# Performance work log

Measured on AMD Instinct MI355X. Metric: run time of the kernel, lower is better.

## Reference

```python
import jax, jax.numpy as jnp
import numpy as np

N = 50000
E = 1600000
IN_C = 128
HID = 64
OUT_C = 64
EPS = 1e-5
NEG_SLOPE = 0.01  # nn.LeakyReLU default


def setup_inputs() -> dict:
    key = jax.random.key(0)
    ks = jax.random.split(key, 8)
    x = jax.random.normal(ks[0], (N, IN_C), dtype=jnp.float32)
    x_e = jnp.zeros((1,), dtype=jnp.float32)  # unused by the module
    edge_index = jax.random.randint(ks[1], (2, E), 0, N, dtype=jnp.int64)
    # Parameters (torch default-ish init scale)
    s1 = 1.0 / np.sqrt(IN_C)
    W1 = jax.random.uniform(ks[2], (HID, IN_C), jnp.float32, -s1, s1)
    b1 = jax.random.uniform(ks[3], (HID,), jnp.float32, -s1, s1)
    gamma = jnp.ones((HID,), jnp.float32)
    beta = jnp.zeros((HID,), jnp.float32)
    s2 = 1.0 / np.sqrt(HID)
    W2 = jax.random.uniform(ks[4], (OUT_C, HID), jnp.float32, -s2, s2)
    b2 = jax.random.uniform(ks[5], (OUT_C,), jnp.float32, -s2, s2)
    return {"x": x, "x_e": x_e, "edge_index": edge_index,
            "W1": W1, "b1": b1, "gamma": gamma, "beta": beta,
            "W2": W2, "b2": b2}


def reference(x, x_e, edge_index, W1, b1, gamma, beta, W2, b2):
    # dropout: identity in eval mode
    h = jax.nn.leaky_relu(x @ W1.T + b1, negative_slope=NEG_SLOPE)  # [N, HID]
    # LayerNorm over last dim
    mu = jnp.mean(h, axis=-1, keepdims=True)
    var = jnp.mean(jnp.square(h - mu), axis=-1, keepdims=True)
    h = (h - mu) * jax.lax.rsqrt(var + EPS) * gamma + beta
    # gather over src edges, scatter-min into dst nodes
    src, dst = edge_index[0], edge_index[1]
    agg = jax.ops.segment_min(h[src], dst, num_segments=N)  # [N, HID]
    # nodes with no incoming edge: segment_min -> +inf; PyG fills 0
    agg = jnp.where(jnp.isinf(agg), 0.0, agg)
    out = agg @ W2.T + b2  # [N, OUT_C]
    return out
```

## Files before the change

kernel.cpp:

```cpp
#include <hip/hip_runtime.h>
#include <hip/hip_fp16.h>
#include <cstdint>
#include <math.h>

#define IN_C 128
#define HID 64
#define OUT_C 64
#define EPS_LN 1e-5f
#define NEG_SLOPE 0.01f

#define NBUCKET 1024
#define ROWS 49
#define CAP 2048
#define EPB 4096

typedef __attribute__((ext_vector_type(8))) short short8;
typedef __attribute__((ext_vector_type(4))) float f32x4;
typedef __attribute__((ext_vector_type(2))) _Float16 f16x2;
typedef __attribute__((ext_vector_type(8))) _Float16 f16x8;

__device__ __forceinline__ unsigned pack_hi(float f0, float f1) {
    return (__float_as_uint(f0) >> 16) | (__float_as_uint(f1) & 0xFFFF0000u);
}
__device__ __forceinline__ float hi_part(float f) {
    return __uint_as_float(__float_as_uint(f) & 0xFFFF0000u);
}
__device__ __forceinline__ unsigned hmin2u(unsigned a, unsigned b) {
    union { unsigned u; f16x2 v; } ua, ub, r;
    ua.u = a; ub.u = b;
    r.v = __builtin_elementwise_min(ua.v, ub.v);
    return r.u;
}

__global__ __launch_bounds__(512) void mlp_and_scatter_kernel(
    const float* __restrict__ x, const float* __restrict__ W1,
    const float* __restrict__ b1, const float* __restrict__ gamma,
    const float* __restrict__ beta, unsigned short* __restrict__ h16,
    const int* __restrict__ ei, unsigned* __restrict__ cursor ,
    unsigned* __restrict__ pairs, int N, int E, int NB_MLP, int NB_SCAT)
{
    __shared__ __align__(16) unsigned smem[12928];

    const int tid = threadIdx.x;
    const int bx  = blockIdx.x;

    const int nmin2 = 2 * min(NB_MLP, NB_SCAT);
    bool do_mlp; int id;
    if (bx < nmin2) { do_mlp = (bx & 1) == 0; id = bx >> 1; }
    else {
        int rr = bx - nmin2;
        do_mlp = (NB_MLP > NB_SCAT);
        id = (nmin2 >> 1) + rr;
    }

    if (do_mlp) {
        unsigned* whi = smem;
        unsigned* wlo = smem + 4352;
        unsigned short* hT = (unsigned short*)(smem + 8704);

        if (tid < 256) {
            int r = tid >> 2, q = tid & 3;
            const float4* wr4 = (const float4*)(W1 + r * IN_C + q * 32);
#pragma unroll
            for (int p = 0; p < 8; ++p) {
                float4 f = wr4[p];
                whi[r * 68 + q * 16 + 2 * p]     = pack_hi(f.x, f.y);
                whi[r * 68 + q * 16 + 2 * p + 1] = pack_hi(f.z, f.w);
                wlo[r * 68 + q * 16 + 2 * p]     = pack_hi(f.x - hi_part(f.x), f.y - hi_part(f.y));
                wlo[r * 68 + q * 16 + 2 * p + 1] = pack_hi(f.z - hi_part(f.z), f.w - hi_part(f.w));
            }
        }
        __syncthreads();

        const int lane = tid & 63;
        const int w    = tid >> 6;
        const int col  = lane & 15;
        const int g    = lane >> 4;
        const int nodeBase0 = id * 128;
        const int nodeBase  = nodeBase0 + w * 16;

        f32x4 acc[4];
#pragma unroll
        for (int t = 0; t < 4; ++t) acc[t] = (f32x4){0.f, 0.f, 0.f, 0.f};

        const int nodeCl = min(nodeBase + col, N - 1);

#pragma unroll
        for (int ks = 0; ks < 4; ++ks) {
            const float* xp = x + (size_t)nodeCl * IN_C + ks * 32 + g * 8;
            float4 fa = *(const float4*)xp;
            float4 fb = *(const float4*)(xp + 4);
            float f[8] = {fa.x, fa.y, fa.z, fa.w, fb.x, fb.y, fb.z, fb.w};
            union { unsigned u[4]; short8 s; } Ah, Al;
#pragma unroll
            for (int p = 0; p < 4; ++p) {
                float f0 = f[2 * p], f1 = f[2 * p + 1];
                Ah.u[p] = pack_hi(f0, f1);
                Al.u[p] = pack_hi(f0 - hi_part(f0), f1 - hi_part(f1));
            }
#pragma unroll
            for (int t = 0; t < 4; ++t) {
                short8 Bh = *(const short8*)&whi[(t * 16 + col) * 68 + ks * 16 + g * 4];
                short8 Bl = *(const short8*)&wlo[(t * 16 + col) * 68 + ks * 16 + g * 4];
                acc[t] = __builtin_amdgcn_mfma_f32_16x16x32_bf16(Ah.s, Bh, acc[t], 0, 0, 0);
                acc[t] = __builtin_amdgcn_mfma_f32_16x16x32_bf16(Ah.s, Bl, acc[t], 0, 0, 0);
                acc[t] = __builtin_amdgcn_mfma_f32_16x16x32_bf16(Al.s, Bh, acc[t], 0, 0, 0);
            }
        }

        float b1v[4], gv[4], bv[4];
#pragma unroll
        for (int t = 0; t < 4; ++t) {
            b1v[t] = b1[t * 16 + col];
            gv[t]  = gamma[t * 16 + col];
            bv[t]  = beta[t * 16 + col];
        }
        float val[4][4];
#pragma unroll
        for (int t = 0; t < 4; ++t)
#pragma unroll
            for (int r = 0; r < 4; ++r) {
                float v = acc[t][r] + b1v[t];
                val[t][r] = v > 0.f ? v : v * NEG_SLOPE;
            }

        float s[4], q[4];
#pragma unroll
        for (int r = 0; r < 4; ++r) {
            s[r] = val[0][r] + val[1][r] + val[2][r] + val[3][r];
            q[r] = fmaf(val[0][r], val[0][r],
                   fmaf(val[1][r], val[1][r],
                   fmaf(val[2][r], val[2][r], val[3][r] * val[3][r])));
        }
#pragma unroll
        for (int off = 1; off < 16; off <<= 1) {
#pragma unroll
            for (int r = 0; r < 4; ++r) {
                s[r] += __shfl_xor(s[r], off, 64);
                q[r] += __shfl_xor(q[r], off, 64);
            }
        }
        float mu[4], rstd[4];
#pragma unroll
        for (int r = 0; r < 4; ++r) {
            mu[r] = s[r] * (1.f / 64.f);
            float var = q[r] * (1.f / 64.f) - mu[r] * mu[r];
            rstd[r] = rsqrtf(var + EPS_LN);
        }
#pragma unroll
        for (int t = 0; t < 4; ++t)
#pragma unroll
            for (int r = 0; r < 4; ++r) {
                float hn = (val[t][r] - mu[r]) * rstd[r] * gv[t] + bv[t];
                int nodeL = w * 16 + g * 4 + r;
                hT[nodeL * 66 + t * 16 + col] = __half_as_ushort(__float2half(hn));
            }
        __syncthreads();

        {
            int nodeL = tid >> 2, part = tid & 3;
            int node = nodeBase0 + nodeL;
            if (node < N) {
                const unsigned* hrow = (const unsigned*)hT;
                unsigned tmp[8];
#pragma unroll
                for (int i = 0; i < 8; ++i) tmp[i] = hrow[nodeL * 33 + part * 8 + i];
                unsigned* gp = (unsigned*)h16 + (size_t)node * 32 + part * 8;
                *(uint4*)gp       = (uint4){tmp[0], tmp[1], tmp[2], tmp[3]};
                *(uint4*)(gp + 4) = (uint4){tmp[4], tmp[5], tmp[6], tmp[7]};
            }
        }
    } else {
        unsigned* staged    = smem;
        unsigned short* bof = (unsigned short*)(smem + 4096);
        unsigned* hist      = smem + 6144;
        unsigned* run_start = smem + 7168;
        unsigned* c2        = smem + 8192;
        unsigned* gbase     = smem + 9216;
        unsigned* wsum      = smem + 10240;

        const int base = id * EPB;
        const int lane = tid & 63;
        const int wv   = tid >> 6;

        hist[tid] = 0;
        hist[tid + 512] = 0;
        __syncthreads();

        unsigned pk[8];
        unsigned short bk[8];
#pragma unroll
        for (int k = 0; k < 8; ++k) {
            int e = base + k * 512 + tid;
            if (e < E) {
                unsigned src = (unsigned)ei[e];
                unsigned dst = (unsigned)ei[E + e];
                unsigned b = dst & (NBUCKET - 1);
                pk[k] = src | ((dst >> 10) << 16);
                bk[k] = (unsigned short)b;
                atomicAdd(&hist[b], 1u);
            } else {
                bk[k] = 0xFFFFu;
            }
        }
        __syncthreads();

        unsigned sA = hist[2 * tid], sB = hist[2 * tid + 1];
        unsigned sv = sA + sB;
        unsigned inc = sv;
#pragma unroll
        for (int off = 1; off < 64; off <<= 1) {
            unsigned u = __shfl_up(inc, (unsigned)off, 64);
            if (lane >= off) inc += u;
        }
        if (lane == 63) wsum[wv] = inc;
        __syncthreads();
        unsigned wbase = 0;
        for (int i = 0; i < wv; ++i) wbase += wsum[i];
        unsigned excl = wbase + inc - sv;

        run_start[2 * tid] = excl;
        run_start[2 * tid + 1] = excl + sA;
        c2[2 * tid] = excl;
        c2[2 * tid + 1] = excl + sA;
        if (sA) gbase[2 * tid] = atomicAdd(&cursor[(2 * tid) * 16], sA);
        if (sB) gbase[2 * tid + 1] = atomicAdd(&cursor[(2 * tid + 1) * 16], sB);
        __syncthreads();

#pragma unroll
        for (int k = 0; k < 8; ++k) {
            if (bk[k] != 0xFFFFu) {
                unsigned pos = atomicAdd(&c2[bk[k]], 1u);
                staged[pos] = pk[k];
                bof[pos] = bk[k];
            }
        }
        __syncthreads();

        int total = min(EPB, E - base);
        for (int i = tid; i < total; i += 512) {
            unsigned b = bof[i];
            unsigned local = gbase[b] + ((unsigned)i - run_start[b]);
            if (local < CAP) pairs[(size_t)b * CAP + local] = staged[i];
        }
    }
}

__global__ __launch_bounds__(512) void bucket_reduce_gemm_kernel(
    const unsigned* __restrict__ hp ,
    const unsigned* __restrict__ cursor, const unsigned* __restrict__ pairs,
    const float* __restrict__ W2, const float* __restrict__ b2,
    float* __restrict__ out, int N)
{
    __shared__ unsigned rec_sorted[CAP];
    __shared__ unsigned accP[64 * 36];
    __shared__ unsigned w2h[64 * 36];
    __shared__ unsigned rhist[64], rstart[64], rc[64];

    const int tid  = threadIdx.x;
    const int lane = tid & 63;
    const int wid  = tid >> 6;
    const unsigned b = blockIdx.x;
    const unsigned INITV = 0x7C007C00u;

    if (tid < 64) rhist[tid] = 0;
    for (int i = tid; i < 64 * 36; i += 512) accP[i] = INITV;
    for (int i = tid; i < 64 * 32; i += 512) {
        int n = i >> 5, p = i & 31;
        float f0 = W2[n * 64 + 2 * p], f1 = W2[n * 64 + 2 * p + 1];
        unsigned u0 = (unsigned)__half_as_ushort(__float2half(f0));
        unsigned u1 = (unsigned)__half_as_ushort(__float2half(f1));
        w2h[n * 36 + p] = u0 | (u1 << 16);
    }

    const unsigned cnt = min(cursor[b * 16], (unsigned)CAP);
    unsigned myrec[4];
#pragma unroll
    for (int k = 0; k < 4; ++k) {
        unsigned i = (unsigned)tid + k * 512;
        myrec[k] = (i < cnt) ? pairs[(size_t)b * CAP + i] : 0xFFFFFFFFu;
    }
    __syncthreads();

#pragma unroll
    for (int k = 0; k < 4; ++k)
        if (myrec[k] != 0xFFFFFFFFu) atomicAdd(&rhist[myrec[k] >> 16], 1u);
    __syncthreads();

    if (wid == 0) {
        unsigned v = (lane < ROWS) ? rhist[lane] : 0u;
        unsigned inc = v;
#pragma unroll
        for (int off = 1; off < 64; off <<= 1) {
            unsigned u = __shfl_up(inc, (unsigned)off, 64);
            if (lane >= off) inc += u;
        }
        if (lane < ROWS) { rstart[lane] = inc - v; rc[lane] = inc - v; }
    }
    __syncthreads();

#pragma unroll
    for (int k = 0; k < 4; ++k)
        if (myrec[k] != 0xFFFFFFFFu) {
            unsigned pos = atomicAdd(&rc[myrec[k] >> 16], 1u);
            rec_sorted[pos] = myrec[k];
        }
    __syncthreads();

    const unsigned sub = (unsigned)(lane >> 3);
    const unsigned cg  = (unsigned)(lane & 7);
    for (int r = wid; r < ROWS; r += 8) {
        unsigned L = rhist[r];
        if (L == 0) continue;
        unsigned st = rstart[r];
        uint4 acc  = {INITV, INITV, INITV, INITV};
        uint4 acc2 = {INITV, INITV, INITV, INITV};
        for (unsigned bb = 0; bb < L; bb += 16) {
            unsigned k1 = min(bb + sub, L - 1);
            unsigned k2 = min(bb + 8 + sub, L - 1);
            unsigned n1 = rec_sorted[st + k1] & 0xFFFFu;
            unsigned n2 = rec_sorted[st + k2] & 0xFFFFu;
            uint4 v1 = *(const uint4*)(hp + (size_t)n1 * 32 + cg * 4);
            uint4 v2 = *(const uint4*)(hp + (size_t)n2 * 32 + cg * 4);
            acc.x  = hmin2u(acc.x,  v1.x); acc.y  = hmin2u(acc.y,  v1.y);
            acc.z  = hmin2u(acc.z,  v1.z); acc.w  = hmin2u(acc.w,  v1.w);
            acc2.x = hmin2u(acc2.x, v2.x); acc2.y = hmin2u(acc2.y, v2.y);
            acc2.z = hmin2u(acc2.z, v2.z); acc2.w = hmin2u(acc2.w, v2.w);
        }
        acc.x = hmin2u(acc.x, acc2.x); acc.y = hmin2u(acc.y, acc2.y);
        acc.z = hmin2u(acc.z, acc2.z); acc.w = hmin2u(acc.w, acc2.w);
#pragma unroll
        for (int off = 8; off < 64; off <<= 1) {
            acc.x = hmin2u(acc.x, (unsigned)__shfl_xor((int)acc.x, off, 64));
            acc.y = hmin2u(acc.y, (unsigned)__shfl_xor((int)acc.y, off, 64));
            acc.z = hmin2u(acc.z, (unsigned)__shfl_xor((int)acc.z, off, 64));
            acc.w = hmin2u(acc.w, (unsigned)__shfl_xor((int)acc.w, off, 64));
        }
        if (lane < 8)
            *(uint4*)&accP[r * 36 + cg * 4] = acc;
    }
    __syncthreads();

    for (int i = tid; i < 64 * 32; i += 512) {
        int r = i >> 5, p = i & 31;
        unsigned v = accP[r * 36 + p];
        unsigned lo = v & 0xFFFFu, hi = v >> 16;
        if (lo == 0x7C00u) lo = 0;
        if (hi == 0x7C00u) hi = 0;
        accP[r * 36 + p] = lo | (hi << 16);
    }
    __syncthreads();

    {
        const int col = lane & 15;
        const int g   = lane >> 4;
        const int mtile = wid >> 1;
        f16x8 afrag[2];
#pragma unroll
        for (int kt = 0; kt < 2; ++kt)
            afrag[kt] = *(const f16x8*)&accP[(mtile * 16 + col) * 36 + kt * 16 + g * 4];
#pragma unroll
        for (int nn = 0; nn < 2; ++nn) {
            int ntile = (wid & 1) * 2 + nn;
            f16x8 b0  = *(const f16x8*)&w2h[(ntile * 16 + col) * 36 + 0 * 16 + g * 4];
            f16x8 b1f = *(const f16x8*)&w2h[(ntile * 16 + col) * 36 + 1 * 16 + g * 4];
            f32x4 c = {0.f, 0.f, 0.f, 0.f};
            c = __builtin_amdgcn_mfma_f32_16x16x32_f16(afrag[0], b0, c, 0, 0, 0);
            c = __builtin_amdgcn_mfma_f32_16x16x32_f16(afrag[1], b1f, c, 0, 0, 0);
            float b2v = b2[ntile * 16 + col];
#pragma unroll
            for (int r4 = 0; r4 < 4; ++r4) {
                int m = mtile * 16 + g * 4 + r4;
                int dst = (m << 10) | (int)b;
                if (m < ROWS && dst < N)
                    out[(size_t)dst * OUT_C + ntile * 16 + col] = c[r4] + b2v;
            }
        }
    }
}

extern "C" void kernel_launch(void* const* d_in, const int* in_sizes, int n_in,
                              void* d_out, int out_size, void* d_ws, size_t ws_size,
                              hipStream_t stream) {
    const float* x     = (const float*)d_in[0];
    const int*   ei    = (const int*)d_in[2];
    const float* W1    = (const float*)d_in[3];
    const float* b1    = (const float*)d_in[4];
    const float* gamma = (const float*)d_in[5];
    const float* beta  = (const float*)d_in[6];
    const float* W2    = (const float*)d_in[7];
    const float* b2    = (const float*)d_in[8];
    float* out = (float*)d_out;

    const int N = in_sizes[0] / IN_C;
    const int E = in_sizes[2] / 2;

    unsigned short* h16 = (unsigned short*)d_ws;
    unsigned* pairs  = (unsigned*)(h16 + (size_t)N * HID);
    unsigned* cursor = pairs + (size_t)NBUCKET * CAP;

    hipMemsetAsync(cursor, 0, (size_t)NBUCKET * 16 * sizeof(unsigned), stream);

    const int NB_MLP  = (N + 127) / 128;
    const int NB_SCAT = (E + EPB - 1) / EPB;
    mlp_and_scatter_kernel<<<NB_MLP + NB_SCAT, 512, 0, stream>>>(
        x, W1, b1, gamma, beta, h16, ei, cursor, pairs, N, E, NB_MLP, NB_SCAT);

    bucket_reduce_gemm_kernel<<<NBUCKET, 512, 0, stream>>>(
        (const unsigned*)h16, cursor, pairs, W2, b2, out, N);
}
```

Baseline: 141.7 us.

## Pack full dst into edge records, shrink LDS, and unroll gather-min four ways

Edge records now store the full destination index in the upper 16 bits, so the bucket id is recovered from the record itself and the separate per-edge bucket array in shared memory is dropped. The MLP path reuses the weight LDS region for its transposed output, guarded by an extra barrier, cutting LDS per block to allow more resident blocks. The reduce kernel derives the row from the top bits and unrolls the gather-min loop to four independent accumulators for more memory-level parallelism. The packing assumes node indices fit the bit layout (src under 65536, dst under 2^22), which holds for N=50000.

```diff
diff --git a/kernel.cpp b/kernel.cpp
--- a/kernel.cpp
+++ b/kernel.cpp
@@ -30,6 +30,11 @@
     ua.u = a; ub.u = b;
     r.v = __builtin_elementwise_min(ua.v, ub.v);
     return r.u;
+}
+__device__ __forceinline__ uint4 min4(uint4 a, uint4 b) {
+    a.x = hmin2u(a.x, b.x); a.y = hmin2u(a.y, b.y);
+    a.z = hmin2u(a.z, b.z); a.w = hmin2u(a.w, b.w);
+    return a;
 }
 
 __global__ __launch_bounds__(512) void mlp_and_scatter_kernel(
@@ -39,7 +44,7 @@
     const int* __restrict__ ei, unsigned* __restrict__ cursor ,
     unsigned* __restrict__ pairs, int N, int E, int NB_MLP, int NB_SCAT)
 {
-    __shared__ __align__(16) unsigned smem[12928];
+    __shared__ __align__(16) unsigned smem[8704];
 
     const int tid = threadIdx.x;
     const int bx  = blockIdx.x;
@@ -56,7 +61,7 @@
     if (do_mlp) {
         unsigned* whi = smem;
         unsigned* wlo = smem + 4352;
-        unsigned short* hT = (unsigned short*)(smem + 8704);
+        unsigned short* hT = (unsigned short*)smem;
 
         if (tid < 256) {
             int r = tid >> 2, q = tid & 3;
@@ -147,6 +152,8 @@
             float var = q[r] * (1.f / 64.f) - mu[r] * mu[r];
             rstd[r] = rsqrtf(var + EPS_LN);
         }
+
+        __syncthreads();
 #pragma unroll
         for (int t = 0; t < 4; ++t)
 #pragma unroll
@@ -172,12 +179,11 @@
         }
     } else {
         unsigned* staged    = smem;
-        unsigned short* bof = (unsigned short*)(smem + 4096);
-        unsigned* hist      = smem + 6144;
-        unsigned* run_start = smem + 7168;
-        unsigned* c2        = smem + 8192;
-        unsigned* gbase     = smem + 9216;
-        unsigned* wsum      = smem + 10240;
+        unsigned* hist      = smem + 4096;
+        unsigned* run_start = smem + 5120;
+        unsigned* c2        = smem + 6144;
+        unsigned* gbase     = smem + 7168;
+        unsigned* wsum      = smem + 8192;
 
         const int base = id * EPB;
         const int lane = tid & 63;
@@ -196,7 +202,7 @@
                 unsigned src = (unsigned)ei[e];
                 unsigned dst = (unsigned)ei[E + e];
                 unsigned b = dst & (NBUCKET - 1);
-                pk[k] = src | ((dst >> 10) << 16);
+                pk[k] = src | (dst << 16);
                 bk[k] = (unsigned short)b;
                 atomicAdd(&hist[b], 1u);
             } else {
@@ -232,16 +238,16 @@
             if (bk[k] != 0xFFFFu) {
                 unsigned pos = atomicAdd(&c2[bk[k]], 1u);
                 staged[pos] = pk[k];
-                bof[pos] = bk[k];
             }
         }
         __syncthreads();
 
         int total = min(EPB, E - base);
         for (int i = tid; i < total; i += 512) {
-            unsigned b = bof[i];
+            unsigned rec = staged[i];
+            unsigned b = (rec >> 16) & (NBUCKET - 1);
             unsigned local = gbase[b] + ((unsigned)i - run_start[b]);
-            if (local < CAP) pairs[(size_t)b * CAP + local] = staged[i];
+            if (local < CAP) pairs[(size_t)b * CAP + local] = rec;
         }
     }
 }
@@ -284,7 +290,7 @@
 
 #pragma unroll
     for (int k = 0; k < 4; ++k)
-        if (myrec[k] != 0xFFFFFFFFu) atomicAdd(&rhist[myrec[k] >> 16], 1u);
+        if (myrec[k] != 0xFFFFFFFFu) atomicAdd(&rhist[myrec[k] >> 26], 1u);
     __syncthreads();
 
     if (wid == 0) {
@@ -302,7 +308,7 @@
 #pragma unroll
     for (int k = 0; k < 4; ++k)
         if (myrec[k] != 0xFFFFFFFFu) {
-            unsigned pos = atomicAdd(&rc[myrec[k] >> 16], 1u);
+            unsigned pos = atomicAdd(&rc[myrec[k] >> 26], 1u);
             rec_sorted[pos] = myrec[k];
         }
     __syncthreads();
@@ -313,22 +319,25 @@
         unsigned L = rhist[r];
         if (L == 0) continue;
         unsigned st = rstart[r];
-        uint4 acc  = {INITV, INITV, INITV, INITV};
-        uint4 acc2 = {INITV, INITV, INITV, INITV};
-        for (unsigned bb = 0; bb < L; bb += 16) {
-            unsigned k1 = min(bb + sub, L - 1);
-            unsigned k2 = min(bb + 8 + sub, L - 1);
+        uint4 a0 = {INITV, INITV, INITV, INITV};
+        uint4 a1 = a0, a2 = a0, a3 = a0;
+        for (unsigned bb = 0; bb < L; bb += 32) {
+            unsigned k0 = min(bb + sub,      L - 1);
+            unsigned k1 = min(bb + 8 + sub,  L - 1);
+            unsigned k2 = min(bb + 16 + sub, L - 1);
+            unsigned k3 = min(bb + 24 + sub, L - 1);
+            unsigned n0 = rec_sorted[st + k0] & 0xFFFFu;
             unsigned n1 = rec_sorted[st + k1] & 0xFFFFu;
             unsigned n2 = rec_sorted[st + k2] & 0xFFFFu;
+            unsigned n3 = rec_sorted[st + k3] & 0xFFFFu;
+            uint4 v0 = *(const uint4*)(hp + (size_t)n0 * 32 + cg * 4);
             uint4 v1 = *(const uint4*)(hp + (size_t)n1 * 32 + cg * 4);
             uint4 v2 = *(const uint4*)(hp + (size_t)n2 * 32 + cg * 4);
-            acc.x  = hmin2u(acc.x,  v1.x); acc.y  = hmin2u(acc.y,  v1.y);
-            acc.z  = hmin2u(acc.z,  v1.z); acc.w  = hmin2u(acc.w,  v1.w);
-            acc2.x = hmin2u(acc2.x, v2.x); acc2.y = hmin2u(acc2.y, v2.y);
-            acc2.z = hmin2u(acc2.z, v2.z); acc2.w = hmin2u(acc2.w, v2.w);
-        }
-        acc.x = hmin2u(acc.x, acc2.x); acc.y = hmin2u(acc.y, acc2.y);
-        acc.z = hmin2u(acc.z, acc2.z); acc.w = hmin2u(acc.w, acc2.w);
+            uint4 v3 = *(const uint4*)(hp + (size_t)n3 * 32 + cg * 4);
+            a0 = min4(a0, v0); a1 = min4(a1, v1);
+            a2 = min4(a2, v2); a3 = min4(a3, v3);
+        }
+        uint4 acc = min4(min4(a0, a1), min4(a2, a3));
 #pragma unroll
         for (int off = 8; off < 64; off <<= 1) {
             acc.x = hmin2u(acc.x, (unsigned)__shfl_xor((int)acc.x, off, 64));
```

After: 143.8 us. No clear change (+1.5%).
